# Kernel tuning notes

Measured on AMD Instinct MI355X. Metric: run time of the kernel, lower is better.

## Reference

```python
import jax, jax.numpy as jnp
import numpy as np

B, H, W, C = 4, 64, 64, 512
DQK = C // 8


def setup_inputs() -> dict:
    key = jax.random.key(0)
    k1, k2, k3, k4 = jax.random.split(key, 4)
    x = jax.random.normal(k1, (B, H, W, C), dtype=jnp.float32)
    kernel_f = jax.random.normal(k2, (1, 1, C, DQK), dtype=jnp.float32) * 0.02
    kernel_g = jax.random.normal(k3, (1, 1, C, DQK), dtype=jnp.float32) * 0.02
    kernel_h = jax.random.normal(k4, (1, 1, C, C), dtype=jnp.float32) * 0.02
    gamma = jnp.ones((1,), dtype=jnp.float32)  # nonzero so attention branch contributes
    return {"x": x, "kernel_f": kernel_f, "kernel_g": kernel_g,
            "kernel_h": kernel_h, "gamma": gamma}


def reference(x, kernel_f, kernel_g, kernel_h, gamma):
    b, h, w, c = x.shape
    n = h * w
    xt = x.reshape(b, n, c)  # 1x1 conv == per-pixel matmul
    f = jnp.einsum('bnc,cd->bnd', xt, kernel_f[0, 0])       # [b,n,dqk]
    g = jnp.einsum('bnc,cd->bnd', xt, kernel_g[0, 0])       # [b,n,dqk]
    v = jnp.einsum('bnc,cd->bnd', xt, kernel_h[0, 0])       # [b,n,c]
    s = jnp.einsum('bid,bjd->bij', f, g)                    # [b,n,n] = f @ g^T
    beta = jax.nn.softmax(s, axis=-1)
    out = jnp.einsum('bij,bjc->bic', beta, v)               # [b,n,c]
    out = out.reshape(b, h, w, c)
    return gamma * out + x
```

## Files before the change

### kernel.cpp

```cpp
#include <hip/hip_runtime.h>


typedef __bf16 bf16x8 __attribute__((ext_vector_type(8)));
typedef __bf16 bf16x2 __attribute__((ext_vector_type(2)));
typedef float f32x4 __attribute__((ext_vector_type(4)));
typedef unsigned int u32x4 __attribute__((ext_vector_type(4)));
typedef unsigned int u32;

#define L2E 1.4426950408889634f

__device__ __forceinline__ unsigned short f2bf(float f) {
    unsigned int u = __builtin_bit_cast(unsigned int, f);
    u += 0x7fffu + ((u >> 16) & 1u);
    return (unsigned short)(u >> 16);
}
__device__ __forceinline__ u32 cvtpk(float a, float b) {
    bf16x2 t; t[0] = (__bf16)a; t[1] = (__bf16)b;
    return __builtin_bit_cast(u32, t);
}
__device__ __forceinline__ bf16x8 ld8(const void* p) {
    u32x4 u = *reinterpret_cast<const u32x4*>(p);
    return __builtin_bit_cast(bf16x8, u);
}
__device__ __forceinline__ bf16x8 ldx(const float* p) {
    float4 a = *reinterpret_cast<const float4*>(p);
    float4 b = *reinterpret_cast<const float4*>(p + 4);
    u32x4 r;
    r.x = cvtpk(a.x, a.y); r.y = cvtpk(a.z, a.w);
    r.z = cvtpk(b.x, b.y); r.w = cvtpk(b.z, b.w);
    return __builtin_bit_cast(bf16x8, r);
}
__device__ __forceinline__ f32x4 mfma16(bf16x8 a, bf16x8 b, f32x4 c) {
    return __builtin_amdgcn_mfma_f32_16x16x32_bf16(a, b, c, 0, 0, 0);
}
__device__ __forceinline__ void gl2lds16(const void* g, void* l) {
    __builtin_amdgcn_global_load_lds(
        (const __attribute__((address_space(1))) u32*)g,
        (__attribute__((address_space(3))) u32*)l, 16, 0, 0);
}

__global__ __launch_bounds__(256) void cvt_w_all(const float* __restrict__ kf,
                                                 const float* __restrict__ kg,
                                                 const float* __restrict__ kh,
                                                 unsigned short* __restrict__ wst) {
    int idx = blockIdx.x * 256 + threadIdx.x;
    int j = idx & 7;
    int gi = idx >> 3;
    int c = gi % 640;
    int sq = gi / 640;
    int k = (sq >> 2) * 32 + (sq & 3) * 8 + j;
    float v;
    if (c < 64)       v = kf[k * 64 + c] * L2E;
    else if (c < 128) v = kg[k * 64 + (c - 64)];
    else              v = kh[k * 512 + (c - 128)];
    wst[idx] = f2bf(v);
}

__global__ __launch_bounds__(256, 2) void proj_k(const float* __restrict__ x,
                                                 const unsigned short* __restrict__ wst,
                                                 unsigned short* __restrict__ fq,
                                                 unsigned short* __restrict__ kst,
                                                 unsigned short* __restrict__ vst) {
    __shared__ __align__(16) unsigned char Wl[2][20480];
    __shared__ unsigned short Tl[64][72];

    int m0 = blockIdx.x * 64;
    int grp = blockIdx.y;
    int tid = threadIdx.x;
    int w = tid >> 6, l = tid & 63, g = l >> 4, i = l & 15;

    const char* wsrc = (const char*)wst + (size_t)w * 10240 + (size_t)grp * 5120 + l * 16;

#pragma unroll
    for (int s5 = 0; s5 < 5; s5++)
        gl2lds16(wsrc + s5 * 1024, &Wl[0][w * 5120 + s5 * 1024]);

    const float* xrow = x + (size_t)(m0 + 16 * w + i) * 512 + g * 8;
    bf16x8 af[16];
#pragma unroll
    for (int k = 0; k < 16; k++) af[k] = ldx(xrow + 32 * k);

    f32x4 acc[5][4];
#pragma unroll
    for (int t = 0; t < 5; t++)
#pragma unroll
        for (int cf = 0; cf < 4; cf++) acc[t][cf] = f32x4{0, 0, 0, 0};

    int rdoff = g * 5120 + i * 16;

#pragma unroll
    for (int q = 0; q < 16; q++) {
        __syncthreads();
        if (q < 15) {
            const char* src = wsrc + (size_t)(q + 1) * 40960;
#pragma unroll
            for (int s5 = 0; s5 < 5; s5++)
                gl2lds16(src + s5 * 1024, &Wl[(q + 1) & 1][w * 5120 + s5 * 1024]);
        }
        const unsigned char* Wb = &Wl[q & 1][0];
        __builtin_amdgcn_s_setprio(1);
#pragma unroll
        for (int t = 0; t < 5; t++)
#pragma unroll
            for (int cf = 0; cf < 4; cf++) {
                bf16x8 bb = ld8(Wb + rdoff + (t * 64 + 16 * cf) * 16);
                acc[t][cf] = mfma16(af[q], bb, acc[t][cf]);
            }
        __builtin_amdgcn_s_setprio(0);
    }

    int batch = m0 >> 12;
    int kt = (m0 & 4095) >> 6;
    unsigned short* kbase = kst + (size_t)batch * 262144 + (size_t)kt * 4096;
    unsigned short* vbase = vst + (size_t)batch * 2097152 + (size_t)kt * 32768;

#pragma unroll
    for (int t = 0; t < 5; t++) {
        if (grp == 0 && t == 0) {
#pragma unroll
            for (int cf = 0; cf < 4; cf++)
#pragma unroll
                for (int r = 0; r < 4; r++)
                    fq[(size_t)(m0 + 16 * w + 4 * g + r) * 64 + 16 * cf + i] =
                        f2bf(acc[t][cf][r]);
        } else {
            __syncthreads();
#pragma unroll
            for (int cf = 0; cf < 4; cf++) {
                ushort4 v4;
                v4.x = f2bf(acc[t][cf][0]); v4.y = f2bf(acc[t][cf][1]);
                v4.z = f2bf(acc[t][cf][2]); v4.w = f2bf(acc[t][cf][3]);
                *reinterpret_cast<ushort4*>(&Tl[16 * cf + i][16 * w + 4 * g]) = v4;
            }
            __syncthreads();
            if (grp == 0 && t == 1) {
#pragma unroll
                for (int ch = tid; ch < 512; ch += 256) {
                    int jf2 = ch >> 7, ks = (ch >> 6) & 1, l2 = ch & 63;
                    int g2 = l2 >> 4, i2 = l2 & 15;
                    ushort4 o0, o1;
                    o0.x = Tl[ks * 32 + 8 * g2 + 0][16 * jf2 + i2];
                    o0.y = Tl[ks * 32 + 8 * g2 + 1][16 * jf2 + i2];
                    o0.z = Tl[ks * 32 + 8 * g2 + 2][16 * jf2 + i2];
                    o0.w = Tl[ks * 32 + 8 * g2 + 3][16 * jf2 + i2];
                    o1.x = Tl[ks * 32 + 8 * g2 + 4][16 * jf2 + i2];
                    o1.y = Tl[ks * 32 + 8 * g2 + 5][16 * jf2 + i2];
                    o1.z = Tl[ks * 32 + 8 * g2 + 6][16 * jf2 + i2];
                    o1.w = Tl[ks * 32 + 8 * g2 + 7][16 * jf2 + i2];
                    unsigned short* dst = kbase + (size_t)(jf2 * 1024 + ks * 512 + l2 * 8);
                    *reinterpret_cast<ushort4*>(dst)     = o0;
                    *reinterpret_cast<ushort4*>(dst + 4) = o1;
                }
            } else {
                int n0 = (grp == 0) ? (t - 2) * 64 : 192 + t * 64;
#pragma unroll
                for (int ch = tid; ch < 512; ch += 256) {
                    int cc = ch >> 7, ks = (ch >> 6) & 1, l2 = ch & 63;
                    int g2 = l2 >> 4, i2 = l2 & 15;
                    int row = cc * 16 + i2;
                    int jb = 32 * ks + 4 * g2;
                    ushort4 o0, o1;
                    o0.x = Tl[row][jb + 0];  o0.y = Tl[row][jb + 1];
                    o0.z = Tl[row][jb + 2];  o0.w = Tl[row][jb + 3];
                    o1.x = Tl[row][jb + 16]; o1.y = Tl[row][jb + 17];
                    o1.z = Tl[row][jb + 18]; o1.w = Tl[row][jb + 19];
                    int c16 = (n0 >> 4) + cc;
                    unsigned short* dst = vbase + (size_t)(c16 * 1024 + ks * 512 + l2 * 8);
                    *reinterpret_cast<ushort4*>(dst)     = o0;
                    *reinterpret_cast<ushort4*>(dst + 4) = o1;
                }
            }
        }
    }
}

__global__ __launch_bounds__(512, 2) void attn_k(const unsigned short* __restrict__ fq,
                                                 const unsigned short* __restrict__ kst,
                                                 const unsigned short* __restrict__ vst,
                                                 const float* __restrict__ x,
                                                 const float* __restrict__ gamma,
                                                 float* __restrict__ out) {
    __shared__ __align__(16) unsigned char Pl[2][8192];
    __shared__ float l_lds[64];

    int bid = blockIdx.x;
    int xcd = bid & 7;
    int batch = xcd >> 1;
    int qidx = ((xcd & 1) << 5) | (bid >> 3);
    int q0 = qidx * 64;

    int tid = threadIdx.x;
    int w = tid >> 6, l = tid & 63, g = l >> 4, i = l & 15;
    int jf = w >> 1, qfh = w & 1;

    if (tid < 64) l_lds[tid] = 0.0f;

    const unsigned short* fqb = fq + (size_t)batch * 4096 * 64;
    const char* kb = (const char*)kst + (size_t)batch * 524288;
    const char* vb = (const char*)vst + (size_t)batch * 4194304;

    bf16x8 aQ[2][2];
#pragma unroll
    for (int qf_l = 0; qf_l < 2; qf_l++)
#pragma unroll
        for (int ks = 0; ks < 2; ks++)
            aQ[qf_l][ks] = ld8(fqb + (size_t)(q0 + 16 * (2 * qfh + qf_l) + i) * 64 +
                               ks * 32 + g * 8);

    f32x4 acc[4][4];
#pragma unroll
    for (int a = 0; a < 4; a++)
#pragma unroll
        for (int b = 0; b < 4; b++) acc[a][b] = f32x4{0, 0, 0, 0};
    float lp[2] = {0.0f, 0.0f};

    int pwoff = ((2 * qfh) * 2 + (jf >> 1)) * 1024 + l * 16 + (jf & 1) * 8;

    bf16x8 kA[2];
    kA[0] = ld8(kb + (size_t)jf * 2048 + l * 16);
    kA[1] = ld8(kb + (size_t)jf * 2048 + 1024 + l * 16);
    {
        f32x4 sacc[2] = {f32x4{0,0,0,0}, f32x4{0,0,0,0}};
#pragma unroll
        for (int qf_l = 0; qf_l < 2; qf_l++) {
            sacc[qf_l] = mfma16(kA[0], aQ[qf_l][0], sacc[qf_l]);
            sacc[qf_l] = mfma16(kA[1], aQ[qf_l][1], sacc[qf_l]);
        }
        kA[0] = ld8(kb + (size_t)(4 + jf) * 2048 + l * 16);
        kA[1] = ld8(kb + (size_t)(4 + jf) * 2048 + 1024 + l * 16);
#pragma unroll
        for (int qf_l = 0; qf_l < 2; qf_l++) {
            float p0 = __builtin_amdgcn_exp2f(sacc[qf_l][0]);
            float p1 = __builtin_amdgcn_exp2f(sacc[qf_l][1]);
            float p2 = __builtin_amdgcn_exp2f(sacc[qf_l][2]);
            float p3 = __builtin_amdgcn_exp2f(sacc[qf_l][3]);
            lp[qf_l] += (p0 + p1) + (p2 + p3);
            uint2 pk2;
            pk2.x = cvtpk(p0, p1);
            pk2.y = cvtpk(p2, p3);
            *reinterpret_cast<uint2*>(&Pl[0][0] + pwoff + qf_l * 2048) = pk2;
        }
    }

    for (int t = 0; t < 64; ++t) {
        __syncthreads();

        bf16x8 vB[4][2];
#pragma unroll
        for (int cf = 0; cf < 4; cf++)
#pragma unroll
            for (int ks = 0; ks < 2; ks++)
                vB[cf][ks] = ld8(vb + (size_t)(t * 32 + w * 4 + cf) * 2048 +
                                 ks * 1024 + l * 16);

        const unsigned char* Pr = &Pl[t & 1][0];
        bf16x8 aP[4][2];
#pragma unroll
        for (int qf = 0; qf < 4; qf++)
#pragma unroll
            for (int ks = 0; ks < 2; ks++)
                aP[qf][ks] = ld8(Pr + (qf * 2 + ks) * 1024 + l * 16);

        f32x4 sacc[2] = {f32x4{0,0,0,0}, f32x4{0,0,0,0}};
#pragma unroll
        for (int qf_l = 0; qf_l < 2; qf_l++) {
            sacc[qf_l] = mfma16(kA[0], aQ[qf_l][0], sacc[qf_l]);
            sacc[qf_l] = mfma16(kA[1], aQ[qf_l][1], sacc[qf_l]);
        }

        {
            int tk = (t + 2) & 63;
            const char* kn = kb + (size_t)(tk * 4 + jf) * 2048;
            kA[0] = ld8(kn + l * 16);
            kA[1] = ld8(kn + 1024 + l * 16);
        }

        __builtin_amdgcn_s_setprio(1);
#pragma unroll
        for (int cf = 0; cf < 4; cf++)
#pragma unroll
            for (int qf = 0; qf < 4; qf++) {
                acc[qf][cf] = mfma16(aP[qf][0], vB[cf][0], acc[qf][cf]);
                acc[qf][cf] = mfma16(aP[qf][1], vB[cf][1], acc[qf][cf]);
            }
        __builtin_amdgcn_s_setprio(0);

        float msk = (t < 63) ? 1.0f : 0.0f;
        unsigned char* Pb = &Pl[(t + 1) & 1][0];
#pragma unroll
        for (int qf_l = 0; qf_l < 2; qf_l++) {
            float p0 = __builtin_amdgcn_exp2f(sacc[qf_l][0]);
            float p1 = __builtin_amdgcn_exp2f(sacc[qf_l][1]);
            float p2 = __builtin_amdgcn_exp2f(sacc[qf_l][2]);
            float p3 = __builtin_amdgcn_exp2f(sacc[qf_l][3]);
            lp[qf_l] += msk * ((p0 + p1) + (p2 + p3));
            uint2 pk2;
            pk2.x = cvtpk(p0, p1);
            pk2.y = cvtpk(p2, p3);
            *reinterpret_cast<uint2*>(Pb + pwoff + qf_l * 2048) = pk2;
        }
    }

#pragma unroll
    for (int qf_l = 0; qf_l < 2; qf_l++) {
        lp[qf_l] += __shfl_xor(lp[qf_l], 16, 64);
        lp[qf_l] += __shfl_xor(lp[qf_l], 32, 64);
    }
    if (g == 0) {
        atomicAdd(&l_lds[16 * (2 * qfh + 0) + i], lp[0]);
        atomicAdd(&l_lds[16 * (2 * qfh + 1) + i], lp[1]);
    }
    __syncthreads();

    float gam = gamma[0];
#pragma unroll
    for (int qf = 0; qf < 4; qf++) {
#pragma unroll
        for (int r = 0; r < 4; r++) {
            float linv = gam / l_lds[16 * qf + 4 * g + r];
            int n = q0 + 16 * qf + 4 * g + r;
            size_t base = ((size_t)batch * 4096 + n) * 512 + 64 * w;
#pragma unroll
            for (int cf = 0; cf < 4; cf++)
                out[base + 16 * cf + i] = acc[qf][cf][r] * linv + x[base + 16 * cf + i];
        }
    }
}


extern "C" void kernel_launch(void* const* d_in, const int* in_sizes, int n_in,
                              void* d_out, int out_size, void* d_ws, size_t ws_size,
                              hipStream_t stream) {
    const float* x = (const float*)d_in[0];
    const float* kf = (const float*)d_in[1];
    const float* kg = (const float*)d_in[2];
    const float* kh = (const float*)d_in[3];
    const float* gamma = (const float*)d_in[4];
    float* out = (float*)d_out;

    char* ws = (char*)d_ws;
    unsigned short* Fq  = (unsigned short*)(ws);
    unsigned short* Kst = (unsigned short*)(ws + 2097152);
    unsigned short* Vst = (unsigned short*)(ws + 4194304);
    unsigned short* Wst = (unsigned short*)(ws + 20971520);

    cvt_w_all<<<1280, 256, 0, stream>>>(kf, kg, kh, Wst);
    proj_k<<<dim3(256, 2), 256, 0, stream>>>(x, Wst, Fq, Kst, Vst);
    attn_k<<<256, 512, 0, stream>>>(Fq, Kst, Vst, x, gamma, out);
}
```

Baseline: 116.8 us.

## Halve attention query tile to 32 rows and double block count

Shrinks each attention block from 64 to 32 query rows and launches 512 blocks instead of 256. Warps are remapped so two query fragments are each split across four key-column warps. Accumulator registers and P shared memory are halved, and launch bounds are raised to allow 4 blocks per CU. The aim is more parallelism and occupancy across the 256 CUs. The cost is that every block rereads all of V and K, doubling that global/L2 traffic, and each barrier now covers fewer MFMAs.

```diff
diff --git a/kernel.cpp b/kernel.cpp
--- a/kernel.cpp
+++ b/kernel.cpp
@@ -174,72 +174,63 @@
     }
 }
 
-__global__ __launch_bounds__(512, 2) void attn_k(const unsigned short* __restrict__ fq,
+__global__ __launch_bounds__(512, 4) void attn_k(const unsigned short* __restrict__ fq,
                                                  const unsigned short* __restrict__ kst,
                                                  const unsigned short* __restrict__ vst,
                                                  const float* __restrict__ x,
                                                  const float* __restrict__ gamma,
                                                  float* __restrict__ out) {
-    __shared__ __align__(16) unsigned char Pl[2][8192];
-    __shared__ float l_lds[64];
+    __shared__ __align__(16) unsigned char Pl[2][4096];
+    __shared__ float l_lds[32];
 
     int bid = blockIdx.x;
     int xcd = bid & 7;
     int batch = xcd >> 1;
-    int qidx = ((xcd & 1) << 5) | (bid >> 3);
-    int q0 = qidx * 64;
+    int qidx = ((xcd & 1) << 6) | (bid >> 3);
+    int q0 = qidx * 32;
 
     int tid = threadIdx.x;
     int w = tid >> 6, l = tid & 63, g = l >> 4, i = l & 15;
-    int jf = w >> 1, qfh = w & 1;
-
-    if (tid < 64) l_lds[tid] = 0.0f;
+    int qf_s = w >> 2, jf = w & 3;
+
+    if (tid < 32) l_lds[tid] = 0.0f;
 
     const unsigned short* fqb = fq + (size_t)batch * 4096 * 64;
     const char* kb = (const char*)kst + (size_t)batch * 524288;
     const char* vb = (const char*)vst + (size_t)batch * 4194304;
 
-    bf16x8 aQ[2][2];
-#pragma unroll
-    for (int qf_l = 0; qf_l < 2; qf_l++)
-#pragma unroll
-        for (int ks = 0; ks < 2; ks++)
-            aQ[qf_l][ks] = ld8(fqb + (size_t)(q0 + 16 * (2 * qfh + qf_l) + i) * 64 +
-                               ks * 32 + g * 8);
-
-    f32x4 acc[4][4];
-#pragma unroll
-    for (int a = 0; a < 4; a++)
+    bf16x8 aQ[2];
+#pragma unroll
+    for (int ks = 0; ks < 2; ks++)
+        aQ[ks] = ld8(fqb + (size_t)(q0 + 16 * qf_s + i) * 64 + ks * 32 + g * 8);
+
+    f32x4 acc[2][4];
+#pragma unroll
+    for (int a = 0; a < 2; a++)
 #pragma unroll
         for (int b = 0; b < 4; b++) acc[a][b] = f32x4{0, 0, 0, 0};
-    float lp[2] = {0.0f, 0.0f};
-
-    int pwoff = ((2 * qfh) * 2 + (jf >> 1)) * 1024 + l * 16 + (jf & 1) * 8;
+    float lp = 0.0f;
+
+    int pwoff = (2 * qf_s + (jf >> 1)) * 1024 + l * 16 + (jf & 1) * 8;
 
     bf16x8 kA[2];
     kA[0] = ld8(kb + (size_t)jf * 2048 + l * 16);
     kA[1] = ld8(kb + (size_t)jf * 2048 + 1024 + l * 16);
     {
-        f32x4 sacc[2] = {f32x4{0,0,0,0}, f32x4{0,0,0,0}};
-#pragma unroll
-        for (int qf_l = 0; qf_l < 2; qf_l++) {
-            sacc[qf_l] = mfma16(kA[0], aQ[qf_l][0], sacc[qf_l]);
-            sacc[qf_l] = mfma16(kA[1], aQ[qf_l][1], sacc[qf_l]);
-        }
+        f32x4 sacc = f32x4{0, 0, 0, 0};
+        sacc = mfma16(kA[0], aQ[0], sacc);
+        sacc = mfma16(kA[1], aQ[1], sacc);
         kA[0] = ld8(kb + (size_t)(4 + jf) * 2048 + l * 16);
         kA[1] = ld8(kb + (size_t)(4 + jf) * 2048 + 1024 + l * 16);
-#pragma unroll
-        for (int qf_l = 0; qf_l < 2; qf_l++) {
-            float p0 = __builtin_amdgcn_exp2f(sacc[qf_l][0]);
-            float p1 = __builtin_amdgcn_exp2f(sacc[qf_l][1]);
-            float p2 = __builtin_amdgcn_exp2f(sacc[qf_l][2]);
-            float p3 = __builtin_amdgcn_exp2f(sacc[qf_l][3]);
-            lp[qf_l] += (p0 + p1) + (p2 + p3);
-            uint2 pk2;
-            pk2.x = cvtpk(p0, p1);
-            pk2.y = cvtpk(p2, p3);
-            *reinterpret_cast<uint2*>(&Pl[0][0] + pwoff + qf_l * 2048) = pk2;
-        }
+        float p0 = __builtin_amdgcn_exp2f(sacc[0]);
+        float p1 = __builtin_amdgcn_exp2f(sacc[1]);
+        float p2 = __builtin_amdgcn_exp2f(sacc[2]);
+        float p3 = __builtin_amdgcn_exp2f(sacc[3]);
+        lp += (p0 + p1) + (p2 + p3);
+        uint2 pk2;
+        pk2.x = cvtpk(p0, p1);
+        pk2.y = cvtpk(p2, p3);
+        *reinterpret_cast<uint2*>(&Pl[0][0] + pwoff) = pk2;
     }
 
     for (int t = 0; t < 64; ++t) {
@@ -254,19 +245,16 @@
                                  ks * 1024 + l * 16);
 
         const unsigned char* Pr = &Pl[t & 1][0];
-        bf16x8 aP[4][2];
-#pragma unroll
-        for (int qf = 0; qf < 4; qf++)
+        bf16x8 aP[2][2];
+#pragma unroll
+        for (int qf = 0; qf < 2; qf++)
 #pragma unroll
             for (int ks = 0; ks < 2; ks++)
                 aP[qf][ks] = ld8(Pr + (qf * 2 + ks) * 1024 + l * 16);
 
-        f32x4 sacc[2] = {f32x4{0,0,0,0}, f32x4{0,0,0,0}};
-#pragma unroll
-        for (int qf_l = 0; qf_l < 2; qf_l++) {
-            sacc[qf_l] = mfma16(kA[0], aQ[qf_l][0], sacc[qf_l]);
-            sacc[qf_l] = mfma16(kA[1], aQ[qf_l][1], sacc[qf_l]);
-        }
+        f32x4 sacc = f32x4{0, 0, 0, 0};
+        sacc = mfma16(kA[0], aQ[0], sacc);
+        sacc = mfma16(kA[1], aQ[1], sacc);
 
         {
             int tk = (t + 2) & 63;
@@ -279,7 +267,7 @@
 #pragma unroll
         for (int cf = 0; cf < 4; cf++)
 #pragma unroll
-            for (int qf = 0; qf < 4; qf++) {
+            for (int qf = 0; qf < 2; qf++) {
                 acc[qf][cf] = mfma16(aP[qf][0], vB[cf][0], acc[qf][cf]);
                 acc[qf][cf] = mfma16(aP[qf][1], vB[cf][1], acc[qf][cf]);
             }
@@ -287,34 +275,27 @@
 
         float msk = (t < 63) ? 1.0f : 0.0f;
         unsigned char* Pb = &Pl[(t + 1) & 1][0];
-#pragma unroll
-        for (int qf_l = 0; qf_l < 2; qf_l++) {
-            float p0 = __builtin_amdgcn_exp2f(sacc[qf_l][0]);
-            float p1 = __builtin_amdgcn_exp2f(sacc[qf_l][1]);
-            float p2 = __builtin_amdgcn_exp2f(sacc[qf_l][2]);
-            float p3 = __builtin_amdgcn_exp2f(sacc[qf_l][3]);
-            lp[qf_l] += msk * ((p0 + p1) + (p2 + p3));
+        {
+            float p0 = __builtin_amdgcn_exp2f(sacc[0]);
+            float p1 = __builtin_amdgcn_exp2f(sacc[1]);
+            float p2 = __builtin_amdgcn_exp2f(sacc[2]);
+            float p3 = __builtin_amdgcn_exp2f(sacc[3]);
+            lp += msk * ((p0 + p1) + (p2 + p3));
             uint2 pk2;
             pk2.x = cvtpk(p0, p1);
             pk2.y = cvtpk(p2, p3);
-            *reinterpret_cast<uint2*>(Pb + pwoff + qf_l * 2048) = pk2;
-        }
-    }
-
-#pragma unroll
-    for (int qf_l = 0; qf_l < 2; qf_l++) {
-        lp[qf_l] += __shfl_xor(lp[qf_l], 16, 64);
-        lp[qf_l] += __shfl_xor(lp[qf_l], 32, 64);
-    }
-    if (g == 0) {
-        atomicAdd(&l_lds[16 * (2 * qfh + 0) + i], lp[0]);
-        atomicAdd(&l_lds[16 * (2 * qfh + 1) + i], lp[1]);
-    }
+            *reinterpret_cast<uint2*>(Pb + pwoff) = pk2;
+        }
+    }
+
+    lp += __shfl_xor(lp, 16, 64);
+    lp += __shfl_xor(lp, 32, 64);
+    if (g == 0) atomicAdd(&l_lds[16 * qf_s + i], lp);
     __syncthreads();
 
     float gam = gamma[0];
 #pragma unroll
-    for (int qf = 0; qf < 4; qf++) {
+    for (int qf = 0; qf < 2; qf++) {
 #pragma unroll
         for (int r = 0; r < 4; r++) {
             float linv = gam / l_lds[16 * qf + 4 * g + r];
@@ -346,5 +327,5 @@
 
     cvt_w_all<<<1280, 256, 0, stream>>>(kf, kg, kh, Wst);
     proj_k<<<dim3(256, 2), 256, 0, stream>>>(x, Wst, Fq, Kst, Vst);
-    attn_k<<<256, 512, 0, stream>>>(Fq, Kst, Vst, x, gamma, out);
-}
+    attn_k<<<512, 512, 0, stream>>>(Fq, Kst, Vst, x, gamma, out);
+}
```

Measured after the change: 144.1 us. 23.3% more time.
